# Kernel optimization log

Hardware: AMD Instinct MI355X
Metric: run time of the kernel (lower is better)

## Reference

```python
import jax, jax.numpy as jnp
import numpy as np

N_NODES = 20000
N_EDGES = 320000
NODE_DIM = 512
HIDDEN = 512
N_GRAPHS = 64


def setup_inputs() -> dict:
    key = jax.random.key(0)
    ks = jax.random.split(key, 12)
    s = 0.02
    return {
        "joint_x": jax.random.normal(ks[0], (N_NODES, NODE_DIM), jnp.float32),
        "joint_edge_index": jax.random.randint(ks[1], (2, N_EDGES), 0, N_NODES, dtype=jnp.int32),
        "joint_batch": jnp.sort(jax.random.randint(ks[2], (N_NODES,), 0, N_GRAPHS, dtype=jnp.int32)),
        "W_g1": jax.random.normal(ks[3], (NODE_DIM, HIDDEN), jnp.float32) * s,
        "b_g1": jnp.zeros((HIDDEN,), jnp.float32),
        "W_g2": jax.random.normal(ks[4], (HIDDEN, HIDDEN), jnp.float32) * s,
        "b_g2": jnp.zeros((HIDDEN,), jnp.float32),
        "W_c1": jax.random.normal(ks[5], (HIDDEN, HIDDEN // 2), jnp.float32) * s,
        "b_c1": jnp.zeros((HIDDEN // 2,), jnp.float32),
        "W_c2": jax.random.normal(ks[6], (HIDDEN // 2, 1), jnp.float32) * s,
        "b_c2": jnp.zeros((1,), jnp.float32),
    }


def _gin_layer(h, src, dst, W, b):
    # GINConv(nn=Linear, eps=0): nn((1+eps)*x_i + sum_{j->i} x_j)
    agg = jax.ops.segment_sum(h[src], dst, num_segments=N_NODES)  # [N, D]
    return (h + agg) @ W + b


def reference(joint_x, joint_edge_index, joint_batch, W_g1, b_g1, W_g2, b_g2, W_c1, b_c1, W_c2, b_c2):
    src, dst = joint_edge_index[0], joint_edge_index[1]
    h = _gin_layer(joint_x, src, dst, W_g1, b_g1)  # [N, HIDDEN]
    h = _gin_layer(h, src, dst, W_g2, b_g2)        # [N, HIDDEN]
    pooled = jax.ops.segment_sum(h, joint_batch, num_segments=N_GRAPHS)  # [G, HIDDEN]
    z = jax.nn.relu(pooled @ W_c1 + b_c1)
    score = z @ W_c2 + b_c2                        # [G, 1]
    return jax.nn.sigmoid(score).squeeze(-1)       # [G]
```

## Files before the change

kernel.cpp:

```cpp
#include <hip/hip_runtime.h>
#include <math.h>

constexpr int N_NODES = 20000;
constexpr int DIM = 512;
constexpr int NG = 64;
constexpr int CAP = 64;
constexpr int KCH = 128;
constexpr int NCHUNK = (N_NODES + KCH - 1) / KCH;
constexpr int RSPLIT = 4;
constexpr int CPS = (NCHUNK + RSPLIT - 1) / RSPLIT;
constexpr int CGS = 32;
constexpr int CSTR = 16;
constexpr int NODE_BLOCKS = (N_NODES + 3) / 4;
constexpr int INIT_BLOCKS = (N_NODES + 255) / 256;
constexpr int GEMM_TILES = 17 * 4;
constexpr int KSPLIT_TILES = GEMM_TILES * 2;
constexpr int PQ_ELEMS = 513 * 256;
constexpr int EPT = 2;
constexpr int EDGE_BLOCKS = (320000 + 256 * EPT - 1) / (256 * EPT);

__device__ __forceinline__ int lower_bound_i(const int* __restrict__ a, int n, int v) {
  int lo = 0, hi = n;
  while (lo < hi) {
    int mid = (lo + hi) >> 1;
    if (a[mid] < v) lo = mid + 1; else hi = mid;
  }
  return lo;
}

__global__ __launch_bounds__(256) void node_init(const int* __restrict__ batch,
                                                 int* __restrict__ cursor,
                                                 float* __restrict__ ng,
                                                 float* __restrict__ cgpad, int n_nodes) {
  int node = blockIdx.x * 256 + threadIdx.x;
  if (node < n_nodes) cursor[(size_t)node * CSTR] = 0;
  if (blockIdx.x == 0 && threadIdx.x < 64) {
    int gg = threadIdx.x;
    int s0 = lower_bound_i(batch, n_nodes, gg);
    int e0 = lower_bound_i(batch, n_nodes, gg + 1);
    ng[gg] = (float)(e0 - s0);
    cgpad[gg * CGS] = 0.f;
  }
}

__device__ void gemm_stack_tile(const float* __restrict__ A0, const float* __restrict__ extra,
                                const float* __restrict__ B, const float* __restrict__ B2,
                                float* __restrict__ C,
                                int N, int K, int R0, int tile, int kbeg, int kend,
                                float* As, float* Bs, int tid) {
  int bm = (tile >> 2) * 32;
  int bn = (tile & 3) * 64;
  int tx = tid & 15;
  int ty = tid >> 4;
  int ar = tid >> 3;
  int ac = (tid & 7) * 2;
  int br = tid >> 4;
  int bc = (tid & 15) * 4;
  float acc[2][4] = {};
  for (int k0 = kbeg; k0 < kend; k0 += 16) {
    int row = bm + ar;
    float2 av = make_float2(0.f, 0.f);
    if (row < R0)       av = *(const float2*)(A0 + (size_t)row * K + k0 + ac);
    else if (row == R0) av = *(const float2*)(extra + k0 + ac);
    As[(ac + 0) * 34 + ar] = av.x;
    As[(ac + 1) * 34 + ar] = av.y;
    size_t boff = (size_t)(k0 + br) * N + bn + bc;
    float4 bv = *(const float4*)(B + boff);
    if (B2) {
      float4 b2 = *(const float4*)(B2 + boff);
      bv.x += b2.x; bv.y += b2.y; bv.z += b2.z; bv.w += b2.w;
    }
    *(float4*)&Bs[br * 68 + bc] = bv;
    __syncthreads();
#pragma unroll
    for (int kk = 0; kk < 16; ++kk) {
      float2 a01 = *(const float2*)&As[kk * 34 + ty * 2];
      float4 b4  = *(const float4*)&Bs[kk * 68 + tx * 4];
      acc[0][0] = fmaf(a01.x, b4.x, acc[0][0]); acc[0][1] = fmaf(a01.x, b4.y, acc[0][1]);
      acc[0][2] = fmaf(a01.x, b4.z, acc[0][2]); acc[0][3] = fmaf(a01.x, b4.w, acc[0][3]);
      acc[1][0] = fmaf(a01.y, b4.x, acc[1][0]); acc[1][1] = fmaf(a01.y, b4.y, acc[1][1]);
      acc[1][2] = fmaf(a01.y, b4.z, acc[1][2]); acc[1][3] = fmaf(a01.y, b4.w, acc[1][3]);
    }
    __syncthreads();
  }
#pragma unroll
  for (int i = 0; i < 2; ++i) {
    int m = bm + ty * 2 + i;
    if (m > R0) continue;
    *(float4*)&C[(size_t)m * N + bn + tx * 4] =
        make_float4(acc[i][0], acc[i][1], acc[i][2], acc[i][3]);
  }
}

__global__ __launch_bounds__(256) void fill_and_Q(const int* __restrict__ srcI,
                                                  const int* __restrict__ dstI,
                                                  const int* __restrict__ batch,
                                                  int* __restrict__ cursor,
                                                  int* __restrict__ edst,
                                                  float* __restrict__ cgpad,
                                                  const float* __restrict__ Wg2,
                                                  const float* __restrict__ bg2,
                                                  const float* __restrict__ Wc1,
                                                  float* __restrict__ Q, int n_edges) {
  __shared__ float As[16 * 34];
  __shared__ float Bs[16 * 68];
  __shared__ int hist[64];
  int b = blockIdx.x;
  int t = threadIdx.x;
  if (b < KSPLIT_TILES) {
    int ks = b & 1;
    int tile = b >> 1;
    gemm_stack_tile(Wg2, bg2, Wc1, nullptr, Q + (size_t)ks * PQ_ELEMS,
                    256, 512, 512, tile, ks * 256, ks * 256 + 256, As, Bs, t);
  } else {
    int eb = b - KSPLIT_TILES;
    if (t < 64) hist[t] = 0;
    __syncthreads();
    int base = eb * (256 * EPT) + t;
    int s[EPT], d[EPT], c[EPT];
    bool v[EPT];
#pragma unroll
    for (int u = 0; u < EPT; ++u) {
      int i = base + u * 256;
      v[u] = i < n_edges;
      s[u] = v[u] ? srcI[i] : 0;
    }
#pragma unroll
    for (int u = 0; u < EPT; ++u) {
      int i = base + u * 256;
      d[u] = v[u] ? dstI[i] : 0;
    }
#pragma unroll
    for (int u = 0; u < EPT; ++u)
      if (v[u]) c[u] = atomicAdd(&cursor[(size_t)s[u] * CSTR], 1);
#pragma unroll
    for (int u = 0; u < EPT; ++u)
      if (v[u]) edst[(size_t)s[u] * CAP + c[u]] = d[u];
#pragma unroll
    for (int u = 0; u < EPT; ++u)
      if (v[u]) atomicAdd(&hist[batch[d[u]]], 1);
    __syncthreads();
    if (t < 64 && hist[t] != 0) atomicAdd(&cgpad[t * CGS], (float)hist[t]);
  }
}

__global__ __launch_bounds__(256) void build_wT(const int* __restrict__ batch,
                                                const int* __restrict__ deg,
                                                const int* __restrict__ edst,
                                                float* __restrict__ wT, int n_nodes) {
  int node = blockIdx.x * 4 + (threadIdx.x >> 6);
  int g = threadIdx.x & 63;
  if (node >= n_nodes) return;
  int end = deg[(size_t)node * CSTR];
  const int* nb = edst + (size_t)node * CAP;
  float acc = (batch[node] == g) ? 1.f : 0.f;
  int i = 0;
  for (; i + 7 < end; i += 8) {
    int d0 = nb[i], d1 = nb[i + 1], d2 = nb[i + 2], d3 = nb[i + 3];
    int d4 = nb[i + 4], d5 = nb[i + 5], d6 = nb[i + 6], d7 = nb[i + 7];
    int b0 = batch[d0], b1 = batch[d1], b2 = batch[d2], b3 = batch[d3];
    int b4 = batch[d4], b5 = batch[d5], b6 = batch[d6], b7 = batch[d7];
    acc += ((float)(b0 == g) + (float)(b1 == g)) + ((float)(b2 == g) + (float)(b3 == g)) +
           ((float)(b4 == g) + (float)(b5 == g)) + ((float)(b6 == g) + (float)(b7 == g));
  }
  for (; i < end; ++i) acc += (float)(batch[nb[i]] == g);
  wT[(size_t)node * 64 + g] = acc;
}

__global__ __launch_bounds__(256) void cT_and_P(const float* __restrict__ wT,
                                                const int* __restrict__ deg,
                                                const int* __restrict__ edst,
                                                float* __restrict__ cT,
                                                const float* __restrict__ Wg1,
                                                const float* __restrict__ bg1,
                                                const float* __restrict__ Q,
                                                float* __restrict__ P, int n_nodes) {
  __shared__ float As[16 * 34];
  __shared__ float Bs[16 * 68];
  int b = blockIdx.x;
  int t = threadIdx.x;
  if (b < KSPLIT_TILES) {
    int ks = b & 1;
    int tile = b >> 1;
    gemm_stack_tile(Wg1, bg1, Q, Q + PQ_ELEMS, P + (size_t)ks * PQ_ELEMS,
                    256, 512, 512, tile, ks * 256, ks * 256 + 256, As, Bs, t);
  } else {
    int node = (b - KSPLIT_TILES) * 4 + (t >> 6);
    int g = t & 63;
    if (node >= n_nodes) return;
    float acc = wT[(size_t)node * 64 + g];
    int end = deg[(size_t)node * CSTR];
    const int* nb = edst + (size_t)node * CAP;
    int i = 0;
    for (; i + 7 < end; i += 8) {
      int d0 = nb[i], d1 = nb[i + 1], d2 = nb[i + 2], d3 = nb[i + 3];
      int d4 = nb[i + 4], d5 = nb[i + 5], d6 = nb[i + 6], d7 = nb[i + 7];
      float v0 = wT[(size_t)d0 * 64 + g], v1 = wT[(size_t)d1 * 64 + g];
      float v2 = wT[(size_t)d2 * 64 + g], v3 = wT[(size_t)d3 * 64 + g];
      float v4 = wT[(size_t)d4 * 64 + g], v5 = wT[(size_t)d5 * 64 + g];
      float v6 = wT[(size_t)d6 * 64 + g], v7 = wT[(size_t)d7 * 64 + g];
      acc += ((v0 + v1) + (v2 + v3)) + ((v4 + v5) + (v6 + v7));
    }
    for (; i + 3 < end; i += 4) {
      int d0 = nb[i], d1 = nb[i + 1], d2 = nb[i + 2], d3 = nb[i + 3];
      acc += wT[(size_t)d0 * 64 + g] + wT[(size_t)d1 * 64 + g] +
             wT[(size_t)d2 * 64 + g] + wT[(size_t)d3 * 64 + g];
    }
    for (; i < end; ++i) acc += wT[(size_t)nb[i] * 64 + g];
    cT[(size_t)node * 64 + g] = acc;
  }
}

__global__ __launch_bounds__(256) void ugemm(const float* __restrict__ x,
                                             const float* __restrict__ cT,
                                             float* __restrict__ Upart) {
  __shared__ float sc[KCH][64];
  int t = threadIdx.x;
  int k0 = blockIdx.y * KCH;
  int kmax = (N_NODES - k0) < KCH ? (N_NODES - k0) : KCH;
  {
    const float4* src = (const float4*)(cT + (size_t)k0 * 64);
    float4* dst = (float4*)(&sc[0][0]);
    int limit4 = kmax * 16;
    for (int i = t; i < limit4; i += 256) dst[i] = src[i];
  }
  __syncthreads();
  int lane = t & 63;
  int slice = t >> 6;
  int n2 = blockIdx.x * 64 + lane;
  const float2* x2 = (const float2*)x;
  float2 acc[16];
#pragma unroll
  for (int j = 0; j < 16; ++j) acc[j] = make_float2(0.f, 0.f);
  for (int kk = 0; kk < kmax; kk += 4) {
    float2 xv[4];
#pragma unroll
    for (int u = 0; u < 4; ++u)
      xv[u] = x2[(size_t)(k0 + kk + u) * 256 + n2];
#pragma unroll
    for (int u = 0; u < 4; ++u) {
      const float4* cp = (const float4*)&sc[kk + u][slice * 16];
      float4 c0 = cp[0], c1 = cp[1], c2 = cp[2], c3 = cp[3];
      float2 xu = xv[u];
      acc[0].x  = fmaf(c0.x, xu.x, acc[0].x);  acc[0].y  = fmaf(c0.x, xu.y, acc[0].y);
      acc[1].x  = fmaf(c0.y, xu.x, acc[1].x);  acc[1].y  = fmaf(c0.y, xu.y, acc[1].y);
      acc[2].x  = fmaf(c0.z, xu.x, acc[2].x);  acc[2].y  = fmaf(c0.z, xu.y, acc[2].y);
      acc[3].x  = fmaf(c0.w, xu.x, acc[3].x);  acc[3].y  = fmaf(c0.w, xu.y, acc[3].y);
      acc[4].x  = fmaf(c1.x, xu.x, acc[4].x);  acc[4].y  = fmaf(c1.x, xu.y, acc[4].y);
      acc[5].x  = fmaf(c1.y, xu.x, acc[5].x);  acc[5].y  = fmaf(c1.y, xu.y, acc[5].y);
      acc[6].x  = fmaf(c1.z, xu.x, acc[6].x);  acc[6].y  = fmaf(c1.z, xu.y, acc[6].y);
      acc[7].x  = fmaf(c1.w, xu.x, acc[7].x);  acc[7].y  = fmaf(c1.w, xu.y, acc[7].y);
      acc[8].x  = fmaf(c2.x, xu.x, acc[8].x);  acc[8].y  = fmaf(c2.x, xu.y, acc[8].y);
      acc[9].x  = fmaf(c2.y, xu.x, acc[9].x);  acc[9].y  = fmaf(c2.y, xu.y, acc[9].y);
      acc[10].x = fmaf(c2.z, xu.x, acc[10].x); acc[10].y = fmaf(c2.z, xu.y, acc[10].y);
      acc[11].x = fmaf(c2.w, xu.x, acc[11].x); acc[11].y = fmaf(c2.w, xu.y, acc[11].y);
      acc[12].x = fmaf(c3.x, xu.x, acc[12].x); acc[12].y = fmaf(c3.x, xu.y, acc[12].y);
      acc[13].x = fmaf(c3.y, xu.x, acc[13].x); acc[13].y = fmaf(c3.y, xu.y, acc[13].y);
      acc[14].x = fmaf(c3.z, xu.x, acc[14].x); acc[14].y = fmaf(c3.z, xu.y, acc[14].y);
      acc[15].x = fmaf(c3.w, xu.x, acc[15].x); acc[15].y = fmaf(c3.w, xu.y, acc[15].y);
    }
  }
  float2* up = (float2*)Upart;
#pragma unroll
  for (int j = 0; j < 16; ++j) {
    int g = slice * 16 + j;
    up[((size_t)blockIdx.y * 64 + g) * 256 + n2] = acc[j];
  }
}

__global__ __launch_bounds__(128) void reduce_U(const float* __restrict__ Upart,
                                                float* __restrict__ Ured) {
  int g = blockIdx.x;
  int s = blockIdx.y;
  int t = threadIdx.x;
  int c0 = s * CPS;
  int c1 = (c0 + CPS < NCHUNK) ? c0 + CPS : NCHUNK;
  const float4* up = (const float4*)Upart;
  float4 acc = make_float4(0.f, 0.f, 0.f, 0.f);
  for (int c = c0; c < c1; ++c) {
    float4 v = up[((size_t)c * 64 + g) * 128 + t];
    acc.x += v.x; acc.y += v.y; acc.z += v.z; acc.w += v.w;
  }
  ((float4*)Ured)[((size_t)s * 64 + g) * 128 + t] = acc;
}

__global__ __launch_bounds__(256) void head(const float* __restrict__ Ured,
                                            const float* __restrict__ P,
                                            const float* __restrict__ Q,
                                            const float* __restrict__ ng,
                                            const float* __restrict__ cgpad,
                                            const float* __restrict__ bc1,
                                            const float* __restrict__ Wc2,
                                            const float* __restrict__ bc2,
                                            float* __restrict__ out) {
  int g = blockIdx.x;
  int j = threadIdx.x;
  const float* Wc0 = P;
  const float* Wc1p = P + (size_t)PQ_ELEMS;
  const float* v1a = P + (size_t)512 * 256;
  const float* v1b = P + (size_t)PQ_ELEMS + (size_t)512 * 256;
  const float* v2a = Q + (size_t)512 * 256;
  const float* v2b = Q + (size_t)PQ_ELEMS + (size_t)512 * 256;
  __shared__ float p[512];
  float s0 = 0.f, s1 = 0.f;
#pragma unroll
  for (int s = 0; s < RSPLIT; ++s) {
    s0 += Ured[((size_t)s * 64 + g) * DIM + j];
    s1 += Ured[((size_t)s * 64 + g) * DIM + 256 + j];
  }
  p[j] = s0;
  p[j + 256] = s1;
  __syncthreads();
  float cg = ng[g] + cgpad[g * CGS];
  float acc = bc1[j] + cg * (v1a[j] + v1b[j]) + ng[g] * (v2a[j] + v2b[j]);
  for (int k = 0; k < 512; ++k) {
    float w = Wc0[k * 256 + j] + Wc1p[k * 256 + j];
    acc = fmaf(p[k], w, acc);
  }
  float z = fmaxf(acc, 0.f);
  float part = z * Wc2[j];
  for (int off = 32; off > 0; off >>= 1) part += __shfl_down(part, off, 64);
  __shared__ float red[4];
  if ((j & 63) == 0) red[j >> 6] = part;
  __syncthreads();
  if (j == 0) {
    float tot = red[0] + red[1] + red[2] + red[3] + bc2[0];
    out[g] = 1.f / (1.f + expf(-tot));
  }
}

extern "C" void kernel_launch(void* const* d_in, const int* in_sizes, int n_in,
                              void* d_out, int out_size, void* d_ws, size_t ws_size,
                              hipStream_t stream) {
  const float* x    = (const float*)d_in[0];
  const int*   ei   = (const int*)d_in[1];
  const int*   batch= (const int*)d_in[2];
  const float* Wg1  = (const float*)d_in[3];
  const float* bg1  = (const float*)d_in[4];
  const float* Wg2  = (const float*)d_in[5];
  const float* bg2  = (const float*)d_in[6];
  const float* Wc1  = (const float*)d_in[7];
  const float* bc1  = (const float*)d_in[8];
  const float* Wc2  = (const float*)d_in[9];
  const float* bc2  = (const float*)d_in[10];
  float* out = (float*)d_out;

  int n_edges = in_sizes[1] / 2;
  int n_nodes = in_sizes[2];
  const int* srcI = ei;
  const int* dstI = ei + n_edges;

  char* ws = (char*)d_ws;
  size_t off = 0;
  auto alloc = [&](size_t bytes) { char* p = ws + off; off += (bytes + 255) & ~(size_t)255; return p; };
  float* wT    = (float*)alloc((size_t)N_NODES * 64 * sizeof(float));
  float* cT    = (float*)alloc((size_t)N_NODES * 64 * sizeof(float));
  float* Upart = (float*)alloc((size_t)NCHUNK * 64 * DIM * sizeof(float));
  float* Ured  = (float*)alloc((size_t)RSPLIT * 64 * DIM * sizeof(float));
  float* Q     = (float*)alloc((size_t)2 * PQ_ELEMS * sizeof(float));
  float* P     = (float*)alloc((size_t)2 * PQ_ELEMS * sizeof(float));
  float* ng    = (float*)alloc(NG * sizeof(float));
  float* cgpad = (float*)alloc(NG * CGS * sizeof(float));
  int* cursor  = (int*)alloc((size_t)N_NODES * CSTR * sizeof(int));
  int* edst    = (int*)alloc((size_t)N_NODES * CAP * sizeof(int));

  node_init<<<INIT_BLOCKS, 256, 0, stream>>>(batch, cursor, ng, cgpad, n_nodes);
  fill_and_Q<<<KSPLIT_TILES + EDGE_BLOCKS, 256, 0, stream>>>(srcI, dstI, batch, cursor, edst,
                                                             cgpad, Wg2, bg2, Wc1, Q, n_edges);
  build_wT<<<NODE_BLOCKS, 256, 0, stream>>>(batch, cursor, edst, wT, n_nodes);
  cT_and_P<<<KSPLIT_TILES + NODE_BLOCKS, 256, 0, stream>>>(wT, cursor, edst, cT,
                                                           Wg1, bg1, Q, P, n_nodes);
  ugemm<<<dim3(4, NCHUNK), 256, 0, stream>>>(x, cT, Upart);
  reduce_U<<<dim3(64, RSPLIT), 128, 0, stream>>>(Upart, Ured);
  head<<<NG, 256, 0, stream>>>(Ured, P, Q, ng, cgpad, bc1, Wc2, bc2, out);
}
```

Baseline: 224.5 us.

## Fuse cT computation into ugemm and merge wT build with P gemm

Moves the wT construction into the kernel that also computes the P gemm tiles, and folds the second-hop cT gather directly into the U gemm kernel, which writes cT into shared memory instead of a global buffer. This drops one kernel launch and the cT round trip through global memory. Chunk size shrinks to 80 nodes with 512-thread blocks, each covering all 512 columns, giving 250 blocks. Reduction split rises to 10 to match the larger chunk count. The trade-off is a larger Upart buffer to reduce, and the gather now runs inside the gemm blocks, which may stall the FMA phase.

```diff
diff --git a/kernel.cpp b/kernel.cpp
--- a/kernel.cpp
+++ b/kernel.cpp
@@ -5,9 +5,9 @@
 constexpr int DIM = 512;
 constexpr int NG = 64;
 constexpr int CAP = 64;
-constexpr int KCH = 128;
+constexpr int KCH = 80;
 constexpr int NCHUNK = (N_NODES + KCH - 1) / KCH;
-constexpr int RSPLIT = 4;
+constexpr int RSPLIT = 10;
 constexpr int CPS = (NCHUNK + RSPLIT - 1) / RSPLIT;
 constexpr int CGS = 32;
 constexpr int CSTR = 16;
@@ -144,33 +144,10 @@
   }
 }
 
-__global__ __launch_bounds__(256) void build_wT(const int* __restrict__ batch,
+__global__ __launch_bounds__(256) void wT_and_P(const int* __restrict__ batch,
                                                 const int* __restrict__ deg,
                                                 const int* __restrict__ edst,
-                                                float* __restrict__ wT, int n_nodes) {
-  int node = blockIdx.x * 4 + (threadIdx.x >> 6);
-  int g = threadIdx.x & 63;
-  if (node >= n_nodes) return;
-  int end = deg[(size_t)node * CSTR];
-  const int* nb = edst + (size_t)node * CAP;
-  float acc = (batch[node] == g) ? 1.f : 0.f;
-  int i = 0;
-  for (; i + 7 < end; i += 8) {
-    int d0 = nb[i], d1 = nb[i + 1], d2 = nb[i + 2], d3 = nb[i + 3];
-    int d4 = nb[i + 4], d5 = nb[i + 5], d6 = nb[i + 6], d7 = nb[i + 7];
-    int b0 = batch[d0], b1 = batch[d1], b2 = batch[d2], b3 = batch[d3];
-    int b4 = batch[d4], b5 = batch[d5], b6 = batch[d6], b7 = batch[d7];
-    acc += ((float)(b0 == g) + (float)(b1 == g)) + ((float)(b2 == g) + (float)(b3 == g)) +
-           ((float)(b4 == g) + (float)(b5 == g)) + ((float)(b6 == g) + (float)(b7 == g));
-  }
-  for (; i < end; ++i) acc += (float)(batch[nb[i]] == g);
-  wT[(size_t)node * 64 + g] = acc;
-}
-
-__global__ __launch_bounds__(256) void cT_and_P(const float* __restrict__ wT,
-                                                const int* __restrict__ deg,
-                                                const int* __restrict__ edst,
-                                                float* __restrict__ cT,
+                                                float* __restrict__ wT,
                                                 const float* __restrict__ Wg1,
                                                 const float* __restrict__ bg1,
                                                 const float* __restrict__ Q,
@@ -188,83 +165,89 @@
     int node = (b - KSPLIT_TILES) * 4 + (t >> 6);
     int g = t & 63;
     if (node >= n_nodes) return;
-    float acc = wT[(size_t)node * 64 + g];
     int end = deg[(size_t)node * CSTR];
     const int* nb = edst + (size_t)node * CAP;
+    float acc = (batch[node] == g) ? 1.f : 0.f;
     int i = 0;
     for (; i + 7 < end; i += 8) {
       int d0 = nb[i], d1 = nb[i + 1], d2 = nb[i + 2], d3 = nb[i + 3];
       int d4 = nb[i + 4], d5 = nb[i + 5], d6 = nb[i + 6], d7 = nb[i + 7];
+      int b0 = batch[d0], b1 = batch[d1], b2 = batch[d2], b3 = batch[d3];
+      int b4 = batch[d4], b5 = batch[d5], b6 = batch[d6], b7 = batch[d7];
+      acc += ((float)(b0 == g) + (float)(b1 == g)) + ((float)(b2 == g) + (float)(b3 == g)) +
+             ((float)(b4 == g) + (float)(b5 == g)) + ((float)(b6 == g) + (float)(b7 == g));
+    }
+    for (; i < end; ++i) acc += (float)(batch[nb[i]] == g);
+    wT[(size_t)node * 64 + g] = acc;
+  }
+}
+
+__global__ __launch_bounds__(512) void ct_ugemm(const float* __restrict__ wT,
+                                                const int* __restrict__ deg,
+                                                const int* __restrict__ edst,
+                                                const float* __restrict__ x,
+                                                float* __restrict__ Upart, int n_nodes) {
+  __shared__ float scT[KCH][64];
+  int c = blockIdx.x;
+  int t = threadIdx.x;
+  int w = t >> 6;
+  int g = t & 63;
+  int k0 = c * KCH;
+  int kmax = (n_nodes - k0) < KCH ? (n_nodes - k0) : KCH;
+  for (int i = w; i < kmax; i += 8) {
+    int node = k0 + i;
+    float acc = wT[(size_t)node * 64 + g];
+    int end = deg[(size_t)node * CSTR];
+    const int* nb = edst + (size_t)node * CAP;
+    int j = 0;
+    for (; j + 7 < end; j += 8) {
+      int d0 = nb[j], d1 = nb[j + 1], d2 = nb[j + 2], d3 = nb[j + 3];
+      int d4 = nb[j + 4], d5 = nb[j + 5], d6 = nb[j + 6], d7 = nb[j + 7];
       float v0 = wT[(size_t)d0 * 64 + g], v1 = wT[(size_t)d1 * 64 + g];
       float v2 = wT[(size_t)d2 * 64 + g], v3 = wT[(size_t)d3 * 64 + g];
       float v4 = wT[(size_t)d4 * 64 + g], v5 = wT[(size_t)d5 * 64 + g];
       float v6 = wT[(size_t)d6 * 64 + g], v7 = wT[(size_t)d7 * 64 + g];
       acc += ((v0 + v1) + (v2 + v3)) + ((v4 + v5) + (v6 + v7));
     }
-    for (; i + 3 < end; i += 4) {
-      int d0 = nb[i], d1 = nb[i + 1], d2 = nb[i + 2], d3 = nb[i + 3];
+    for (; j + 3 < end; j += 4) {
+      int d0 = nb[j], d1 = nb[j + 1], d2 = nb[j + 2], d3 = nb[j + 3];
       acc += wT[(size_t)d0 * 64 + g] + wT[(size_t)d1 * 64 + g] +
              wT[(size_t)d2 * 64 + g] + wT[(size_t)d3 * 64 + g];
     }
-    for (; i < end; ++i) acc += wT[(size_t)nb[i] * 64 + g];
-    cT[(size_t)node * 64 + g] = acc;
-  }
-}
-
-__global__ __launch_bounds__(256) void ugemm(const float* __restrict__ x,
-                                             const float* __restrict__ cT,
-                                             float* __restrict__ Upart) {
-  __shared__ float sc[KCH][64];
-  int t = threadIdx.x;
-  int k0 = blockIdx.y * KCH;
-  int kmax = (N_NODES - k0) < KCH ? (N_NODES - k0) : KCH;
-  {
-    const float4* src = (const float4*)(cT + (size_t)k0 * 64);
-    float4* dst = (float4*)(&sc[0][0]);
-    int limit4 = kmax * 16;
-    for (int i = t; i < limit4; i += 256) dst[i] = src[i];
+    for (; j < end; ++j) acc += wT[(size_t)nb[j] * 64 + g];
+    scT[i][g] = acc;
   }
   __syncthreads();
-  int lane = t & 63;
-  int slice = t >> 6;
-  int n2 = blockIdx.x * 64 + lane;
   const float2* x2 = (const float2*)x;
-  float2 acc[16];
-#pragma unroll
-  for (int j = 0; j < 16; ++j) acc[j] = make_float2(0.f, 0.f);
-  for (int kk = 0; kk < kmax; kk += 4) {
+  float2 acc[8][4];
+#pragma unroll
+  for (int q = 0; q < 8; ++q)
+#pragma unroll
+    for (int u = 0; u < 4; ++u) acc[q][u] = make_float2(0.f, 0.f);
+#pragma unroll 2
+  for (int kk = 0; kk < kmax; ++kk) {
     float2 xv[4];
 #pragma unroll
     for (int u = 0; u < 4; ++u)
-      xv[u] = x2[(size_t)(k0 + kk + u) * 256 + n2];
-#pragma unroll
-    for (int u = 0; u < 4; ++u) {
-      const float4* cp = (const float4*)&sc[kk + u][slice * 16];
-      float4 c0 = cp[0], c1 = cp[1], c2 = cp[2], c3 = cp[3];
-      float2 xu = xv[u];
-      acc[0].x  = fmaf(c0.x, xu.x, acc[0].x);  acc[0].y  = fmaf(c0.x, xu.y, acc[0].y);
-      acc[1].x  = fmaf(c0.y, xu.x, acc[1].x);  acc[1].y  = fmaf(c0.y, xu.y, acc[1].y);
-      acc[2].x  = fmaf(c0.z, xu.x, acc[2].x);  acc[2].y  = fmaf(c0.z, xu.y, acc[2].y);
-      acc[3].x  = fmaf(c0.w, xu.x, acc[3].x);  acc[3].y  = fmaf(c0.w, xu.y, acc[3].y);
-      acc[4].x  = fmaf(c1.x, xu.x, acc[4].x);  acc[4].y  = fmaf(c1.x, xu.y, acc[4].y);
-      acc[5].x  = fmaf(c1.y, xu.x, acc[5].x);  acc[5].y  = fmaf(c1.y, xu.y, acc[5].y);
-      acc[6].x  = fmaf(c1.z, xu.x, acc[6].x);  acc[6].y  = fmaf(c1.z, xu.y, acc[6].y);
-      acc[7].x  = fmaf(c1.w, xu.x, acc[7].x);  acc[7].y  = fmaf(c1.w, xu.y, acc[7].y);
-      acc[8].x  = fmaf(c2.x, xu.x, acc[8].x);  acc[8].y  = fmaf(c2.x, xu.y, acc[8].y);
-      acc[9].x  = fmaf(c2.y, xu.x, acc[9].x);  acc[9].y  = fmaf(c2.y, xu.y, acc[9].y);
-      acc[10].x = fmaf(c2.z, xu.x, acc[10].x); acc[10].y = fmaf(c2.z, xu.y, acc[10].y);
-      acc[11].x = fmaf(c2.w, xu.x, acc[11].x); acc[11].y = fmaf(c2.w, xu.y, acc[11].y);
-      acc[12].x = fmaf(c3.x, xu.x, acc[12].x); acc[12].y = fmaf(c3.x, xu.y, acc[12].y);
-      acc[13].x = fmaf(c3.y, xu.x, acc[13].x); acc[13].y = fmaf(c3.y, xu.y, acc[13].y);
-      acc[14].x = fmaf(c3.z, xu.x, acc[14].x); acc[14].y = fmaf(c3.z, xu.y, acc[14].y);
-      acc[15].x = fmaf(c3.w, xu.x, acc[15].x); acc[15].y = fmaf(c3.w, xu.y, acc[15].y);
-    }
+      xv[u] = x2[(size_t)(k0 + kk) * 256 + g + u * 64];
+    const float4* cp = (const float4*)&scT[kk][w * 8];
+    float4 cA = cp[0], cB = cp[1];
+    float cv[8] = {cA.x, cA.y, cA.z, cA.w, cB.x, cB.y, cB.z, cB.w};
+#pragma unroll
+    for (int q = 0; q < 8; ++q)
+#pragma unroll
+      for (int u = 0; u < 4; ++u) {
+        acc[q][u].x = fmaf(cv[q], xv[u].x, acc[q][u].x);
+        acc[q][u].y = fmaf(cv[q], xv[u].y, acc[q][u].y);
+      }
   }
   float2* up = (float2*)Upart;
 #pragma unroll
-  for (int j = 0; j < 16; ++j) {
-    int g = slice * 16 + j;
-    up[((size_t)blockIdx.y * 64 + g) * 256 + n2] = acc[j];
+  for (int q = 0; q < 8; ++q) {
+    int gg = w * 8 + q;
+#pragma unroll
+    for (int u = 0; u < 4; ++u)
+      up[((size_t)c * 64 + gg) * 256 + g + u * 64] = acc[q][u];
   }
 }
 
@@ -354,7 +337,6 @@
   size_t off = 0;
   auto alloc = [&](size_t bytes) { char* p = ws + off; off += (bytes + 255) & ~(size_t)255; return p; };
   float* wT    = (float*)alloc((size_t)N_NODES * 64 * sizeof(float));
-  float* cT    = (float*)alloc((size_t)N_NODES * 64 * sizeof(float));
   float* Upart = (float*)alloc((size_t)NCHUNK * 64 * DIM * sizeof(float));
   float* Ured  = (float*)alloc((size_t)RSPLIT * 64 * DIM * sizeof(float));
   float* Q     = (float*)alloc((size_t)2 * PQ_ELEMS * sizeof(float));
@@ -367,10 +349,9 @@
   node_init<<<INIT_BLOCKS, 256, 0, stream>>>(batch, cursor, ng, cgpad, n_nodes);
   fill_and_Q<<<KSPLIT_TILES + EDGE_BLOCKS, 256, 0, stream>>>(srcI, dstI, batch, cursor, edst,
                                                              cgpad, Wg2, bg2, Wc1, Q, n_edges);
-  build_wT<<<NODE_BLOCKS, 256, 0, stream>>>(batch, cursor, edst, wT, n_nodes);
-  cT_and_P<<<KSPLIT_TILES + NODE_BLOCKS, 256, 0, stream>>>(wT, cursor, edst, cT,
+  wT_and_P<<<KSPLIT_TILES + NODE_BLOCKS, 256, 0, stream>>>(batch, cursor, edst, wT,
                                                            Wg1, bg1, Q, P, n_nodes);
-  ugemm<<<dim3(4, NCHUNK), 256, 0, stream>>>(x, cT, Upart);
+  ct_ugemm<<<NCHUNK, 512, 0, stream>>>(wT, cursor, edst, x, Upart, n_nodes);
   reduce_U<<<dim3(64, RSPLIT), 128, 0, stream>>>(Upart, Ured);
   head<<<NG, 256, 0, stream>>>(Ured, P, Q, ng, cgpad, bc1, Wc2, bc2, out);
 }
```

After: 239.4 us. 1.07x slower.
